# Optimization experiments

Measured on AMD Instinct MI355X. Metric: run time of the kernel, lower is better.

The kernel has to match this reference:

```python
import jax, jax.numpy as jnp
import numpy as np

B, N, M = 2, 1024, 512
D, H, DH = 1024, 16, 64          # features, heads, head dim (D == H*DH)
MID = H * DH
DC = 768                          # context_features
MULT = 4
EPS = 1e-5


def _ln(x, w, b):
    mu = jnp.mean(x, -1, keepdims=True)
    var = jnp.mean((x - mu) ** 2, -1, keepdims=True)
    return (x - mu) * jax.lax.rsqrt(var + EPS) * w + b


def _sincos(n, d):
    inv = 1.0 / (10000.0 ** (jnp.arange(0, d, 2, dtype=jnp.float32) / d))
    ang = jnp.arange(n, dtype=jnp.float32)[:, None] * inv[None, :]
    return jnp.sin(ang), jnp.cos(ang)


def _rope(x, sin, cos):
    # x: [B,H,N,DH]; sin/cos: [N, DH//2]; interleaved even/odd rotation
    s = sin[None, None]
    c = cos[None, None]
    xe = x[..., ::2]
    xo = x[..., 1::2]
    re = xe * c - xo * s
    ro = xe * s + xo * c
    return jnp.stack((re, ro), axis=-1).reshape(x.shape)


def _heads(t):
    b, n, _ = t.shape
    return t.reshape(b, n, H, DH).transpose(0, 2, 1, 3)


def _attn(xq, ctx, wq, wkv, wo, bo):
    q = _heads(xq @ wq)
    k, v = jnp.split(ctx @ wkv, 2, axis=-1)
    k = _heads(k)
    v = _heads(v)
    sq, cq = _sincos(q.shape[2], DH)
    sk, ck = _sincos(k.shape[2], DH)
    q = _rope(q, sq, cq)
    k = _rope(k, sk, ck)
    sim = jnp.einsum('bhnd,bhmd->bhnm', q, k) * (DH ** -0.5)
    a = jax.nn.softmax(sim, axis=-1)
    o = jnp.einsum('bhnm,bhmd->bhnd', a, v)
    o = o.transpose(0, 2, 1, 3).reshape(xq.shape[0], xq.shape[1], MID)
    return o @ wo + bo


def _adaln(x, c, lw, lb, gw, gb, bw, bb):
    g = (c @ gw + gb)[:, None, :]
    bt = (c @ bw + bb)[:, None, :]
    return _ln(x, lw, lb) * (1.0 + g) + bt


def setup_inputs() -> dict:
    ks = jax.random.split(jax.random.key(0), 24)
    s = 0.02
    inp = {
        'x': jax.random.normal(ks[0], (B, N, D), jnp.float32),
        'cond': jax.random.normal(ks[1], (B, D), jnp.float32),
        'context': jax.random.normal(ks[2], (B, M, DC), jnp.float32),
        # AdaLN (attn_mod) — reused for self- and cross-attention pre-norm
        'ln1_w': jnp.ones((D,), jnp.float32),
        'ln1_b': jnp.zeros((D,), jnp.float32),
        'g1_w': jax.random.normal(ks[3], (D, D), jnp.float32) * s,
        'g1_b': jnp.zeros((D,), jnp.float32),
        'b1_w': jax.random.normal(ks[4], (D, D), jnp.float32) * s,
        'b1_b': jnp.zeros((D,), jnp.float32),
        # AdaLN (ffn_mod)
        'ln2_w': jnp.ones((D,), jnp.float32),
        'ln2_b': jnp.zeros((D,), jnp.float32),
        'g2_w': jax.random.normal(ks[5], (D, D), jnp.float32) * s,
        'g2_b': jnp.zeros((D,), jnp.float32),
        'b2_w': jax.random.normal(ks[6], (D, D), jnp.float32) * s,
        'b2_b': jnp.zeros((D,), jnp.float32),
        # self-attention
        'sa_wq': jax.random.normal(ks[7], (D, MID), jnp.float32) * s,
        'sa_wkv': jax.random.normal(ks[8], (D, 2 * MID), jnp.float32) * s,
        'sa_wo': jax.random.normal(ks[9], (MID, D), jnp.float32) * s,
        'sa_bo': jnp.zeros((D,), jnp.float32),
        # cross-attention (context LayerNorm + projections)
        'ca_lnc_w': jnp.ones((DC,), jnp.float32),
        'ca_lnc_b': jnp.zeros((DC,), jnp.float32),
        'ca_wq': jax.random.normal(ks[10], (D, MID), jnp.float32) * s,
        'ca_wkv': jax.random.normal(ks[11], (DC, 2 * MID), jnp.float32) * s,
        'ca_wo': jax.random.normal(ks[12], (MID, D), jnp.float32) * s,
        'ca_bo': jnp.zeros((D,), jnp.float32),
        # FFN
        'ff_w1': jax.random.normal(ks[13], (D, MULT * D), jnp.float32) * s,
        'ff_b1': jnp.zeros((MULT * D,), jnp.float32),
        'ff_w2': jax.random.normal(ks[14], (MULT * D, D), jnp.float32) * s,
        'ff_b2': jnp.zeros((D,), jnp.float32),
    }
    return inp


def reference(x, cond, context,
              ln1_w, ln1_b, g1_w, g1_b, b1_w, b1_b,
              ln2_w, ln2_b, g2_w, g2_b, b2_w, b2_b,
              sa_wq, sa_wkv, sa_wo, sa_bo,
              ca_lnc_w, ca_lnc_b, ca_wq, ca_wkv, ca_wo, ca_bo,
              ff_w1, ff_b1, ff_w2, ff_b2):
    # self-attention with shared attn_mod AdaLN
    attn_in = _adaln(x, cond, ln1_w, ln1_b, g1_w, g1_b, b1_w, b1_b)
    x = _attn(attn_in, attn_in, sa_wq, sa_wkv, sa_wo, sa_bo) + x
    # cross-attention (attn_mod reused, context LayerNorm applied)
    cross_in = _adaln(x, cond, ln1_w, ln1_b, g1_w, g1_b, b1_w, b1_b)
    ctx_n = _ln(context, ca_lnc_w, ca_lnc_b)
    x = _attn(cross_in, ctx_n, ca_wq, ca_wkv, ca_wo, ca_bo) + x
    # FFN with ffn_mod AdaLN, exact GELU (torch default)
    ffn_in = _adaln(x, cond, ln2_w, ln2_b, g2_w, g2_b, b2_w, b2_b)
    h = jax.nn.gelu(ffn_in @ ff_w1 + ff_b1, approximate=False)
    x = h @ ff_w2 + ff_b2 + x
    return x
```

## Files before the change

kernel.cpp:

```cpp
#include <hip/hip_runtime.h>
#include <hip/hip_bf16.h>
#include <math.h>


typedef float f32x4 __attribute__((ext_vector_type(4)));
typedef __bf16 bf16x8 __attribute__((ext_vector_type(8)));
typedef __bf16 bf16x4 __attribute__((ext_vector_type(4)));
typedef __bf16 bf16x2 __attribute__((ext_vector_type(2)));

#define DEVI __device__ __forceinline__

DEVI void gload16(const void* g, void* l) {
  __builtin_amdgcn_global_load_lds((const __attribute__((address_space(1))) void*)g,
                                   (__attribute__((address_space(3))) void*)l, 16, 0, 0);
}

struct WtDesc {
  const float* src[8];
  __bf16* dst[8];
  int K[8], N[8];
  int tstart[9];
};

__global__ __launch_bounds__(256) void wt_all_kernel(WtDesc d) {
  __shared__ float tile[32][33];
  int blk = blockIdx.x;
  int e = 0;
#pragma unroll
  for (int i = 0; i < 7; ++i) e += (blk >= d.tstart[i + 1]) ? 1 : 0;
  int li = blk - d.tstart[e];
  const float* W = d.src[e];
  __bf16* WT = d.dst[e];
  int K = d.K[e], N = d.N[e];
  int ntx = N >> 5;
  int n0 = (li % ntx) * 32, k0 = (li / ntx) * 32;
  int tx = threadIdx.x & 31, ty = threadIdx.x >> 5;
#pragma unroll
  for (int i = 0; i < 4; ++i) {
    int k = ty + i * 8;
    tile[k][tx] = W[(size_t)(k0 + k) * N + n0 + tx];
  }
  __syncthreads();
#pragma unroll
  for (int i = 0; i < 4; ++i) {
    int n = ty + i * 8;
    WT[(size_t)(n0 + n) * K + k0 + tx] = (__bf16)tile[tx][n];
  }
}

__global__ __launch_bounds__(256) void mod_part_kernel(
    const float* __restrict__ cond,
    const float* __restrict__ g1w, const float* __restrict__ b1w,
    const float* __restrict__ g2w, const float* __restrict__ b2w,
    float* __restrict__ part) {
  __shared__ float sc[128];
  int dchunk = blockIdx.x, b = blockIdx.y;
  int mat = blockIdx.z >> 3, ks = blockIdx.z & 7;
  const float* W = (mat == 0) ? g1w : (mat == 1) ? b1w : (mat == 2) ? g2w : b2w;
  if (threadIdx.x < 128) sc[threadIdx.x] = cond[b * 1024 + ks * 128 + threadIdx.x];
  __syncthreads();
  int d = dchunk * 256 + threadIdx.x;
  const float* Wp = W + (size_t)(ks * 128) * 1024 + d;
  float acc = 0.f;
#pragma unroll 8
  for (int k = 0; k < 128; ++k) acc += sc[k] * Wp[(size_t)k * 1024];
  part[(size_t)(blockIdx.z * 2 + b) * 1024 + d] = acc;
}

__global__ __launch_bounds__(256) void mod_reduce_kernel(
    const float* __restrict__ part,
    const float* __restrict__ g1b, const float* __restrict__ b1b,
    const float* __restrict__ g2b, const float* __restrict__ b2b,
    float* __restrict__ mods) {
  int idx = blockIdx.x * 256 + threadIdx.x;
  int mat = idx >> 11, b = (idx >> 10) & 1, d = idx & 1023;
  float s = 0.f;
#pragma unroll
  for (int ks = 0; ks < 8; ++ks) s += part[(size_t)((mat * 8 + ks) * 2 + b) * 1024 + d];
  const float* Bv = (mat == 0) ? g1b : (mat == 1) ? b1b : (mat == 2) ? g2b : b2b;
  mods[(size_t)(mat * 2 + b) * 1024 + d] = s + Bv[d];
}

__global__ __launch_bounds__(256) void adaln_kernel(const float* __restrict__ X,
                                                    const float* __restrict__ lnw,
                                                    const float* __restrict__ lnb,
                                                    const float* __restrict__ mods,
                                                    int gi, int bi,
                                                    __bf16* __restrict__ out) {
  __shared__ float red[2][4];
  int row = blockIdx.x;
  int b = row >> 10;
  int t = threadIdx.x;
  const float4 xv = ((const float4*)(X + (size_t)row * 1024))[t];
  float s  = xv.x + xv.y + xv.z + xv.w;
  float s2 = xv.x * xv.x + xv.y * xv.y + xv.z * xv.z + xv.w * xv.w;
  int lane = t & 63, w = t >> 6;
#pragma unroll
  for (int off = 32; off > 0; off >>= 1) {
    s += __shfl_down(s, off);
    s2 += __shfl_down(s2, off);
  }
  if (lane == 0) { red[0][w] = s; red[1][w] = s2; }
  __syncthreads();
  s  = red[0][0] + red[0][1] + red[0][2] + red[0][3];
  s2 = red[1][0] + red[1][1] + red[1][2] + red[1][3];
  float mu = s * (1.0f / 1024.0f);
  float var = s2 * (1.0f / 1024.0f) - mu * mu;
  float rstd = rsqrtf(var + 1e-5f);
  const float4 wv = ((const float4*)lnw)[t];
  const float4 bv = ((const float4*)lnb)[t];
  const float4 gv = ((const float4*)(mods + (size_t)(gi * 2 + b) * 1024))[t];
  const float4 tv = ((const float4*)(mods + (size_t)(bi * 2 + b) * 1024))[t];
  bf16x4 ov;
  ov[0] = (__bf16)(((xv.x - mu) * rstd * wv.x + bv.x) * (1.0f + gv.x) + tv.x);
  ov[1] = (__bf16)(((xv.y - mu) * rstd * wv.y + bv.y) * (1.0f + gv.y) + tv.y);
  ov[2] = (__bf16)(((xv.z - mu) * rstd * wv.z + bv.z) * (1.0f + gv.z) + tv.z);
  ov[3] = (__bf16)(((xv.w - mu) * rstd * wv.w + bv.w) * (1.0f + gv.w) + tv.w);
  *(bf16x4*)(out + (size_t)row * 1024 + t * 4) = ov;
}

__global__ __launch_bounds__(256) void ctxln_kernel(const float* __restrict__ X,
                                                    const float* __restrict__ w,
                                                    const float* __restrict__ bias,
                                                    __bf16* __restrict__ out) {
  __shared__ float red[2][4];
  int row = blockIdx.x;
  int t = threadIdx.x;
  const float* xp = X + (size_t)row * 768;
  float v[3];
  float s = 0.f, s2 = 0.f;
#pragma unroll
  for (int i = 0; i < 3; ++i) {
    v[i] = xp[t + i * 256];
    s += v[i];
    s2 += v[i] * v[i];
  }
  int lane = t & 63, wv_ = t >> 6;
#pragma unroll
  for (int off = 32; off > 0; off >>= 1) {
    s += __shfl_down(s, off);
    s2 += __shfl_down(s2, off);
  }
  if (lane == 0) { red[0][wv_] = s; red[1][wv_] = s2; }
  __syncthreads();
  s  = red[0][0] + red[0][1] + red[0][2] + red[0][3];
  s2 = red[1][0] + red[1][1] + red[1][2] + red[1][3];
  float mu = s * (1.0f / 768.0f);
  float var = s2 * (1.0f / 768.0f) - mu * mu;
  float rstd = rsqrtf(var + 1e-5f);
#pragma unroll
  for (int i = 0; i < 3; ++i) {
    int c = t + i * 256;
    out[(size_t)row * 768 + c] = (__bf16)((v[i] - mu) * rstd * w[c] + bias[c]);
  }
}

__global__ __launch_bounds__(256) void rope_tbl_kernel(float2* __restrict__ tbl) {
  int idx = blockIdx.x * 256 + threadIdx.x;
  int n = idx >> 5, i = idx & 31;
  float inv = expf(-(float)(2 * i) * (1.0f / 64.0f) * 9.210340371976184f);
  float ang = (float)n * inv;
  tbl[idx] = make_float2(sinf(ang), cosf(ang));
}

__global__ __launch_bounds__(256) void vtb_kernel(const __bf16* __restrict__ Vb,
                                                  __bf16* __restrict__ VT, int Ntok) {
  __shared__ __bf16 tile[64][68];
  int bh = blockIdx.x, nt = blockIdx.y;
  int b = bh >> 4, h = bh & 15;
  int t = threadIdx.x;
  int tx = t & 15, ty = t >> 4;
#pragma unroll
  for (int i = 0; i < 4; ++i) {
    int n = ty + i * 16;
    bf16x4 v = *(const bf16x4*)(Vb + (size_t)(b * Ntok + nt * 64 + n) * 1024 + h * 64 + tx * 4);
#pragma unroll
    for (int j = 0; j < 4; ++j) tile[n][tx * 4 + j] = v[j];
  }
  __syncthreads();
#pragma unroll
  for (int i = 0; i < 4; ++i) {
    int d = ty + i * 16;
    bf16x4 o;
#pragma unroll
    for (int j = 0; j < 4; ++j) o[j] = tile[tx * 4 + j][d];
    *(bf16x4*)(VT + ((size_t)bh * 64 + d) * Ntok + nt * 64 + tx * 4) = o;
  }
}

template <int BM, int BN, int EPI, int DEPTH>
__global__ __launch_bounds__(256) void gemm3(const __bf16* __restrict__ A,
                                             const __bf16* __restrict__ BT,
                                             const float* __restrict__ bias,
                                             const float* __restrict__ res,
                                             void* __restrict__ outv,
                                             int M, int N, int K, int kslices,
                                             const float2* __restrict__ tbl,
                                             __bf16* __restrict__ Qro,
                                             __bf16* __restrict__ Kro,
                                             __bf16* __restrict__ Vbo,
                                             int Ntok) {
  constexpr int MI = BM / 32, NI = BN / 32;
  constexpr int NBUF = DEPTH + 1;
  constexpr int LPT = BM / 64 + BN / 64;
  __shared__ __bf16 sA[NBUF][BM * 32];
  __shared__ __bf16 sB[NBUF][BN * 32];
  const int t = threadIdx.x;
  const int w = t >> 6, lane = t & 63;
  const int lr = lane & 15, lg = lane >> 4;
  const int fxor = (lr >> 1) & 3;
  int nwg = gridDim.x * gridDim.y * gridDim.z;
  int flat = blockIdx.x + gridDim.x * (blockIdx.y + gridDim.y * blockIdx.z);
  flat = (flat & 7) * (nwg >> 3) + (flat >> 3);
  const int bm = flat % gridDim.x;
  int rest = flat / gridDim.x;
  const int bn = rest % gridDim.y;
  const int bz = rest / gridDim.y;
  const int wm = (w >> 1) * (BM / 2), wn = (w & 1) * (BN / 2);
  const int kper = K / kslices;
  const int k0 = bz * kper;
  const int nsteps = kper / 32;
  f32x4 acc[MI][NI] = {};

  auto stage = [&](int buf, int kt) {
#pragma unroll
    for (int i = 0; i < BM / 64; ++i) {
      int e8 = i * 256 + t;
      int row = e8 >> 2, c = e8 & 3;
      int scol = (c ^ ((row >> 1) & 3)) << 3;
      gload16(A + (size_t)(bm * BM + row) * K + kt + scol, &sA[buf][e8 * 8]);
    }
#pragma unroll
    for (int i = 0; i < BN / 64; ++i) {
      int e8 = i * 256 + t;
      int row = e8 >> 2, c = e8 & 3;
      int scol = (c ^ ((row >> 1) & 3)) << 3;
      gload16(BT + (size_t)(bn * BN + row) * K + kt + scol, &sB[buf][e8 * 8]);
    }
  };

  auto compute = [&](int buf) {
    bf16x8 af[MI], bfr[NI];
#pragma unroll
    for (int mi = 0; mi < MI; ++mi)
      af[mi] = *(const bf16x8*)(&sA[buf][(wm + mi * 16 + lr) * 32 + ((lg ^ fxor) << 3)]);
#pragma unroll
    for (int ni = 0; ni < NI; ++ni)
      bfr[ni] = *(const bf16x8*)(&sB[buf][(wn + ni * 16 + lr) * 32 + ((lg ^ fxor) << 3)]);
#pragma unroll
    for (int mi = 0; mi < MI; ++mi)
#pragma unroll
      for (int ni = 0; ni < NI; ++ni)
        acc[mi][ni] = __builtin_amdgcn_mfma_f32_16x16x32_bf16(af[mi], bfr[ni], acc[mi][ni], 0, 0, 0);
  };

#pragma unroll
  for (int i = 0; i < DEPTH; ++i) stage(i, k0 + i * 32);

  int it = 0;
  for (; it < nsteps - (DEPTH - 1); ++it) {
    asm volatile("s_waitcnt vmcnt(%0)" :: "n"((DEPTH - 1) * LPT) : "memory");
    __builtin_amdgcn_s_barrier();
    __builtin_amdgcn_sched_barrier(0);
    if (it + DEPTH < nsteps) stage((it + DEPTH) % NBUF, k0 + (it + DEPTH) * 32);
    compute(it % NBUF);
  }
  asm volatile("s_waitcnt vmcnt(0)" ::: "memory");
  __builtin_amdgcn_s_barrier();
  __builtin_amdgcn_sched_barrier(0);
  for (; it < nsteps; ++it) compute(it % NBUF);

#pragma unroll
  for (int mi = 0; mi < MI; ++mi) {
    int row = bm * BM + wm + mi * 16 + lg * 4;
#pragma unroll
    for (int ni = 0; ni < NI; ++ni) {
      int col = bn * BN + wn + ni * 16 + lr;
#pragma unroll
      for (int r = 0; r < 4; ++r) {
        float v = acc[mi][ni][r];
        int erow = row + r;
        size_t off = (size_t)erow * N + col;
        if (EPI == 0) {
          ((float*)outv)[off] = v;
        } else if (EPI == 1) {
          ((float*)outv)[off] = v + bias[col] + res[off];
        } else if (EPI == 2) {
          float xg = v + bias[col];
          ((__bf16*)outv)[off] = (__bf16)(0.5f * xg * (1.0f + erff(xg * 0.7071067811865475f)));
        } else if (EPI == 3) {
          ((float*)outv)[(size_t)bz * M * N + off] = v;
        } else if (EPI == 4) {
          float ov = __shfl_xor(v, 1);
          int b = erow >> 10, n = erow & 1023;
          if (col < 2048) {
            int h = (col >> 6) & 15, dh = col & 63;
            float2 sc = tbl[n * 32 + (dh >> 1)];
            float rv = (lr & 1) ? (ov * sc.x + v * sc.y) : (v * sc.y - ov * sc.x);
            __bf16* dst;
            if (col < 1024) { rv *= 0.125f; dst = Qro; } else dst = Kro;
            dst[((size_t)(b * 16 + h) * Ntok + n) * 64 + dh] = (__bf16)rv;
          } else {
            Vbo[(size_t)erow * 1024 + (col - 2048)] = (__bf16)v;
          }
        } else if (EPI == 5) {
          float ov = __shfl_xor(v, 1);
          int b = erow >> 10, n = erow & 1023;
          int h = col >> 6, dh = col & 63;
          float2 sc = tbl[n * 32 + (dh >> 1)];
          float rv = ((lr & 1) ? (ov * sc.x + v * sc.y) : (v * sc.y - ov * sc.x)) * 0.125f;
          Qro[((size_t)(b * 16 + h) * Ntok + n) * 64 + dh] = (__bf16)rv;
        } else {
          float ov = __shfl_xor(v, 1);
          int b = erow >> 9, n = erow & 511;
          if (col < 1024) {
            int h = col >> 6, dh = col & 63;
            float2 sc = tbl[n * 32 + (dh >> 1)];
            float rv = (lr & 1) ? (ov * sc.x + v * sc.y) : (v * sc.y - ov * sc.x);
            Kro[((size_t)(b * 16 + h) * Ntok + n) * 64 + dh] = (__bf16)rv;
          } else {
            Vbo[(size_t)erow * 1024 + (col - 1024)] = (__bf16)v;
          }
        }
      }
    }
  }
}

__global__ __launch_bounds__(256) void ff2red_kernel(const float* __restrict__ part,
                                                     const float* __restrict__ bias,
                                                     const float* __restrict__ res,
                                                     float* __restrict__ out, int MN, int N) {
  int idx = blockIdx.x * 256 + threadIdx.x;
  float4 p0 = ((const float4*)part)[idx];
  float4 p1 = ((const float4*)(part + MN))[idx];
  float4 rr = ((const float4*)res)[idx];
  int colb = (idx * 4) & (N - 1);
  float4 bb = *(const float4*)(bias + colb);
  float4 o;
  o.x = p0.x + p1.x + bb.x + rr.x;
  o.y = p0.y + p1.y + bb.y + rr.y;
  o.z = p0.z + p1.z + bb.z + rr.z;
  o.w = p0.w + p1.w + bb.w + rr.w;
  ((float4*)out)[idx] = o;
}

template <int KITERS>
__global__ __launch_bounds__(256) void attn_kernel(const __bf16* __restrict__ Qr,
                                                   const __bf16* __restrict__ Kr,
                                                   const __bf16* __restrict__ VT,
                                                   __bf16* __restrict__ O,
                                                   int Nq, int Nk) {
  __shared__ __bf16 sK[2][64 * 64];
  __shared__ __bf16 sV[2][64 * 64];
  __shared__ __bf16 Pl[4][16 * 64];
  const int t = threadIdx.x, w = t >> 6, lane = t & 63;
  const int lr = lane & 15, lg = lane >> 4;
  const int lsrc = lane & 48;
  const int swz = (lr & 7) << 3;
  int flat = blockIdx.x + (blockIdx.y << 4);
  flat = (flat & 7) * 64 + (flat >> 3);
  const int bh = flat >> 4;
  const int q0 = (flat & 15) * 64 + w * 16;
  const int b = bh >> 4, h = bh & 15;

  auto stage = [&](int buf, int kt) {
#pragma unroll
    for (int i = 0; i < 2; ++i) {
      int e8 = i * 256 + t;
      int row = e8 >> 3, col8 = e8 & 7;
      int scol = (col8 ^ (row & 7)) << 3;
      gload16(Kr + ((size_t)bh * Nk + kt + row) * 64 + scol, &sK[buf][e8 * 8]);
      gload16(VT + ((size_t)bh * 64 + row) * Nk + kt + scol, &sV[buf][e8 * 8]);
    }
  };

  bf16x8 qf[2];
#pragma unroll
  for (int kh = 0; kh < 2; ++kh)
    qf[kh] = *(const bf16x8*)(Qr + ((size_t)bh * Nq + q0 + lr) * 64 + kh * 32 + lg * 8);
  f32x4 accO[4] = {};
  float m = -INFINITY, l = 0.f;

  stage(0, 0);
  __syncthreads();
  int cur = 0;
#pragma unroll
  for (int it = 0; it < KITERS; ++it) {
    if (it + 1 < KITERS) stage(cur ^ 1, (it + 1) * 64);
    f32x4 s[4] = {};
#pragma unroll
    for (int nf = 0; nf < 4; ++nf) {
      int r = nf * 16 + lr;
#pragma unroll
      for (int kh = 0; kh < 2; ++kh) {
        bf16x8 kf = *(const bf16x8*)(&sK[cur][r * 64 + (((kh * 4 + lg) ^ (lr & 7)) << 3)]);
        s[nf] = __builtin_amdgcn_mfma_f32_16x16x32_bf16(kf, qf[kh], s[nf], 0, 0, 0);
      }
    }
    float p[16];
#pragma unroll
    for (int j = 0; j < 16; ++j) p[j] = s[j >> 2][j & 3];
    float pm = p[0];
#pragma unroll
    for (int j = 1; j < 16; ++j) pm = fmaxf(pm, p[j]);
    pm = fmaxf(pm, __shfl_xor(pm, 16));
    pm = fmaxf(pm, __shfl_xor(pm, 32));
    if (!__all(pm <= m + 8.f)) {
      float mnew = fmaxf(m, pm);
      float resc = __expf(m - mnew);
      float rq[4];
#pragma unroll
      for (int r = 0; r < 4; ++r) rq[r] = __shfl(resc, lsrc | (lg * 4 + r));
#pragma unroll
      for (int df = 0; df < 4; ++df)
#pragma unroll
        for (int r = 0; r < 4; ++r) accO[df][r] *= rq[r];
      l *= resc;
      m = mnew;
    }
    float rs = 0.f;
#pragma unroll
    for (int j = 0; j < 16; ++j) { p[j] = __expf(p[j] - m); rs += p[j]; }
    rs += __shfl_xor(rs, 16);
    rs += __shfl_xor(rs, 32);
    l += rs;
#pragma unroll
    for (int nf = 0; nf < 4; ++nf)
#pragma unroll
      for (int jj = 0; jj < 2; ++jj) {
        int k = nf * 16 + lg * 4 + 2 * jj;
        bf16x2 pk;
        pk[0] = (__bf16)p[nf * 4 + 2 * jj];
        pk[1] = (__bf16)p[nf * 4 + 2 * jj + 1];
        *(bf16x2*)(&Pl[w][lr * 64 + (k ^ swz)]) = pk;
      }
    bf16x8 pa0 = *(const bf16x8*)(&Pl[w][lr * 64 + ((lg * 8) ^ swz)]);
    bf16x8 pa1 = *(const bf16x8*)(&Pl[w][lr * 64 + ((32 + lg * 8) ^ swz)]);
#pragma unroll
    for (int df = 0; df < 4; ++df) {
      int d = df * 16 + lr;
      bf16x8 vf0 = *(const bf16x8*)(&sV[cur][d * 64 + ((lg ^ (lr & 7)) << 3)]);
      bf16x8 vf1 = *(const bf16x8*)(&sV[cur][d * 64 + (((4 + lg) ^ (lr & 7)) << 3)]);
      accO[df] = __builtin_amdgcn_mfma_f32_16x16x32_bf16(pa0, vf0, accO[df], 0, 0, 0);
      accO[df] = __builtin_amdgcn_mfma_f32_16x16x32_bf16(pa1, vf1, accO[df], 0, 0, 0);
    }
    __syncthreads();
    cur ^= 1;
  }
  float lq[4];
#pragma unroll
  for (int r = 0; r < 4; ++r) lq[r] = __shfl(l, lsrc | (lg * 4 + r));
#pragma unroll
  for (int r = 0; r < 4; ++r) {
    float inv = 1.0f / lq[r];
    int n = q0 + lg * 4 + r;
#pragma unroll
    for (int df = 0; df < 4; ++df)
      O[(size_t)(b * 1024 + n) * 1024 + h * 64 + df * 16 + lr] = (__bf16)(accO[df][r] * inv);
  }
}

extern "C" void kernel_launch(void* const* d_in, const int* in_sizes, int n_in,
                              void* d_out, int out_size, void* d_ws, size_t ws_size,
                              hipStream_t stream) {
  (void)in_sizes; (void)n_in; (void)out_size; (void)ws_size;
  const float* x       = (const float*)d_in[0];
  const float* cond    = (const float*)d_in[1];
  const float* ctx     = (const float*)d_in[2];
  const float* ln1_w   = (const float*)d_in[3];
  const float* ln1_b   = (const float*)d_in[4];
  const float* g1_w    = (const float*)d_in[5];
  const float* g1_b    = (const float*)d_in[6];
  const float* b1_w    = (const float*)d_in[7];
  const float* b1_b    = (const float*)d_in[8];
  const float* ln2_w   = (const float*)d_in[9];
  const float* ln2_b   = (const float*)d_in[10];
  const float* g2_w    = (const float*)d_in[11];
  const float* g2_b    = (const float*)d_in[12];
  const float* b2_w    = (const float*)d_in[13];
  const float* b2_b    = (const float*)d_in[14];
  const float* sa_wq   = (const float*)d_in[15];
  const float* sa_wkv  = (const float*)d_in[16];
  const float* sa_wo   = (const float*)d_in[17];
  const float* sa_bo   = (const float*)d_in[18];
  const float* ca_lnc_w = (const float*)d_in[19];
  const float* ca_lnc_b = (const float*)d_in[20];
  const float* ca_wq   = (const float*)d_in[21];
  const float* ca_wkv  = (const float*)d_in[22];
  const float* ca_wo   = (const float*)d_in[23];
  const float* ca_bo   = (const float*)d_in[24];
  const float* ff_w1   = (const float*)d_in[25];
  const float* ff_b1   = (const float*)d_in[26];
  const float* ff_w2   = (const float*)d_in[27];
  const float* ff_b2   = (const float*)d_in[28];
  float* out = (float*)d_out;

  char* ws = (char*)d_ws;
  size_t o = 0;
  auto alloc = [&](size_t bytes) {
    void* p = ws + o;
    o += (bytes + 255) & ~(size_t)255;
    return p;
  };

  __bf16* wqT   = (__bf16*)alloc(1024ull * 1024 * 2);
  __bf16* wkvT  = (__bf16*)alloc(2048ull * 1024 * 2);
  __bf16* woT   = (__bf16*)alloc(1024ull * 1024 * 2);
  __bf16* cwqT  = (__bf16*)alloc(1024ull * 1024 * 2);
  __bf16* cwkvT = (__bf16*)alloc(2048ull * 768 * 2);
  __bf16* cwoT  = (__bf16*)alloc(1024ull * 1024 * 2);
  __bf16* ff1T  = (__bf16*)alloc(4096ull * 1024 * 2);
  __bf16* ff2T  = (__bf16*)alloc(1024ull * 4096 * 2);
  float*  mods  = (float*)alloc(4ull * 2 * 1024 * 4);
  float2* tbl   = (float2*)alloc(1024ull * 32 * 8);
  __bf16* ain   = (__bf16*)alloc(2048ull * 1024 * 2);
  float*  Qf    = (float*)alloc(2048ull * 1024 * 4);
  float*  KVf   = (float*)alloc(2048ull * 2048 * 4);
  __bf16* ctxn  = (__bf16*)alloc(1024ull * 768 * 2);
  __bf16* Qr    = (__bf16*)alloc(2048ull * 1024 * 2);
  __bf16* Kr    = (__bf16*)alloc(2048ull * 1024 * 2);
  __bf16* VTb   = (__bf16*)alloc(2048ull * 1024 * 2);
  __bf16* Ob    = (__bf16*)alloc(2048ull * 1024 * 2);
  float*  x1    = (float*)alloc(2048ull * 1024 * 4);
  float*  x2    = (float*)alloc(2048ull * 1024 * 4);
  __bf16* hb    = (__bf16*)KVf;
  float*  pbuf  = (float*)Qr;
  float*  mpart = (float*)Qf;
  __bf16* Vb    = (__bf16*)Qf;

  WtDesc wd;
  const float* srcs[8] = {sa_wq, sa_wkv, sa_wo, ca_wq, ca_wkv, ca_wo, ff_w1, ff_w2};
  __bf16* dsts[8] = {wqT, wkvT, woT, cwqT, cwkvT, cwoT, ff1T, ff2T};
  int Ks[8] = {1024, 1024, 1024, 1024, 768, 1024, 1024, 4096};
  int Ns[8] = {1024, 2048, 1024, 1024, 2048, 1024, 4096, 1024};
  int cum = 0;
  for (int i = 0; i < 8; ++i) {
    wd.src[i] = srcs[i]; wd.dst[i] = dsts[i]; wd.K[i] = Ks[i]; wd.N[i] = Ns[i];
    wd.tstart[i] = cum;
    cum += (Ks[i] >> 5) * (Ns[i] >> 5);
  }
  wd.tstart[8] = cum;
  wt_all_kernel<<<cum, 256, 0, stream>>>(wd);
  rope_tbl_kernel<<<128, 256, 0, stream>>>(tbl);
  mod_part_kernel<<<dim3(4, 2, 32), 256, 0, stream>>>(cond, g1_w, b1_w, g2_w, b2_w, mpart);
  mod_reduce_kernel<<<32, 256, 0, stream>>>(mpart, g1_b, b1_b, g2_b, b2_b, mods);

  adaln_kernel<<<2048, 256, 0, stream>>>(x, ln1_w, ln1_b, mods, 0, 1, ain);
  gemm3<128, 128, 4, 3><<<dim3(16, 24), 256, 0, stream>>>(ain, wqT, nullptr, nullptr, nullptr,
                                                          2048, 3072, 1024, 1, tbl, Qr, Kr, Vb, 1024);
  vtb_kernel<<<dim3(32, 16), 256, 0, stream>>>(Vb, VTb, 1024);
  attn_kernel<16><<<dim3(16, 32), 256, 0, stream>>>(Qr, Kr, VTb, Ob, 1024, 1024);
  gemm3<128, 64, 1, 3><<<dim3(16, 16), 256, 0, stream>>>(Ob, woT, sa_bo, x, x1,
                                                         2048, 1024, 1024, 1, nullptr, nullptr, nullptr, nullptr, 0);

  adaln_kernel<<<2048, 256, 0, stream>>>(x1, ln1_w, ln1_b, mods, 0, 1, ain);
  ctxln_kernel<<<1024, 256, 0, stream>>>(ctx, ca_lnc_w, ca_lnc_b, ctxn);
  gemm3<128, 64, 5, 3><<<dim3(16, 16), 256, 0, stream>>>(ain, cwqT, nullptr, nullptr, nullptr,
                                                         2048, 1024, 1024, 1, tbl, Qr, nullptr, nullptr, 1024);
  gemm3<128, 64, 6, 3><<<dim3(8, 32), 256, 0, stream>>>(ctxn, cwkvT, nullptr, nullptr, nullptr,
                                                        1024, 2048, 768, 1, tbl, nullptr, Kr, Vb, 512);
  vtb_kernel<<<dim3(32, 8), 256, 0, stream>>>(Vb, VTb, 512);
  attn_kernel<8><<<dim3(16, 32), 256, 0, stream>>>(Qr, Kr, VTb, Ob, 1024, 512);
  gemm3<128, 64, 1, 3><<<dim3(16, 16), 256, 0, stream>>>(Ob, cwoT, ca_bo, x1, x2,
                                                         2048, 1024, 1024, 1, nullptr, nullptr, nullptr, nullptr, 0);

  adaln_kernel<<<2048, 256, 0, stream>>>(x2, ln2_w, ln2_b, mods, 2, 3, ain);
  gemm3<128, 128, 2, 3><<<dim3(16, 32), 256, 0, stream>>>(ain, ff1T, ff_b1, nullptr, hb,
                                                          2048, 4096, 1024, 1, nullptr, nullptr, nullptr, nullptr, 0);
  gemm3<128, 64, 3, 3><<<dim3(16, 16, 2), 256, 0, stream>>>(hb, ff2T, nullptr, nullptr, pbuf,
                                                            2048, 1024, 4096, 2, nullptr, nullptr, nullptr, nullptr, 0);
  ff2red_kernel<<<2048, 256, 0, stream>>>(pbuf, ff_b2, x2, out, 2048 * 1024, 1024);
}
```

Baseline: 272.1 us.

## Merge prep kernels, fuse cross-attn Q and KV GEMMs, shrink GEMM tiles

```diff
diff --git a/kernel.cpp b/kernel.cpp
--- a/kernel.cpp
+++ b/kernel.cpp
@@ -22,49 +22,60 @@
   int tstart[9];
 };
 
-__global__ __launch_bounds__(256) void wt_all_kernel(WtDesc d) {
-  __shared__ float tile[32][33];
+__global__ __launch_bounds__(256) void prep_kernel(WtDesc d,
+                                                   float2* __restrict__ tbl,
+                                                   const float* __restrict__ cond,
+                                                   const float* __restrict__ g1w,
+                                                   const float* __restrict__ b1w,
+                                                   const float* __restrict__ g2w,
+                                                   const float* __restrict__ b2w,
+                                                   float* __restrict__ part) {
+  __shared__ float smem[32][33];
   int blk = blockIdx.x;
-  int e = 0;
-#pragma unroll
-  for (int i = 0; i < 7; ++i) e += (blk >= d.tstart[i + 1]) ? 1 : 0;
-  int li = blk - d.tstart[e];
-  const float* W = d.src[e];
-  __bf16* WT = d.dst[e];
-  int K = d.K[e], N = d.N[e];
-  int ntx = N >> 5;
-  int n0 = (li % ntx) * 32, k0 = (li / ntx) * 32;
-  int tx = threadIdx.x & 31, ty = threadIdx.x >> 5;
-#pragma unroll
-  for (int i = 0; i < 4; ++i) {
-    int k = ty + i * 8;
-    tile[k][tx] = W[(size_t)(k0 + k) * N + n0 + tx];
-  }
-  __syncthreads();
-#pragma unroll
-  for (int i = 0; i < 4; ++i) {
-    int n = ty + i * 8;
-    WT[(size_t)(n0 + n) * K + k0 + tx] = (__bf16)tile[tx][n];
-  }
-}
-
-__global__ __launch_bounds__(256) void mod_part_kernel(
-    const float* __restrict__ cond,
-    const float* __restrict__ g1w, const float* __restrict__ b1w,
-    const float* __restrict__ g2w, const float* __restrict__ b2w,
-    float* __restrict__ part) {
-  __shared__ float sc[128];
-  int dchunk = blockIdx.x, b = blockIdx.y;
-  int mat = blockIdx.z >> 3, ks = blockIdx.z & 7;
-  const float* W = (mat == 0) ? g1w : (mat == 1) ? b1w : (mat == 2) ? g2w : b2w;
-  if (threadIdx.x < 128) sc[threadIdx.x] = cond[b * 1024 + ks * 128 + threadIdx.x];
-  __syncthreads();
-  int d = dchunk * 256 + threadIdx.x;
-  const float* Wp = W + (size_t)(ks * 128) * 1024 + d;
-  float acc = 0.f;
+  int wtend = d.tstart[8];
+  if (blk < wtend) {
+    int e = 0;
+#pragma unroll
+    for (int i = 0; i < 7; ++i) e += (blk >= d.tstart[i + 1]) ? 1 : 0;
+    int li = blk - d.tstart[e];
+    const float* W = d.src[e];
+    __bf16* WT = d.dst[e];
+    int K = d.K[e], N = d.N[e];
+    int ntx = N >> 5;
+    int n0 = (li % ntx) * 32, k0 = (li / ntx) * 32;
+    int tx = threadIdx.x & 31, ty = threadIdx.x >> 5;
+#pragma unroll
+    for (int i = 0; i < 4; ++i) {
+      int k = ty + i * 8;
+      smem[k][tx] = W[(size_t)(k0 + k) * N + n0 + tx];
+    }
+    __syncthreads();
+#pragma unroll
+    for (int i = 0; i < 4; ++i) {
+      int n = ty + i * 8;
+      WT[(size_t)(n0 + n) * K + k0 + tx] = (__bf16)smem[tx][n];
+    }
+  } else if (blk < wtend + 128) {
+    int idx = (blk - wtend) * 256 + threadIdx.x;
+    int n = idx >> 5, i = idx & 31;
+    float inv = expf(-(float)(2 * i) * (1.0f / 64.0f) * 9.210340371976184f);
+    float ang = (float)n * inv;
+    tbl[idx] = make_float2(sinf(ang), cosf(ang));
+  } else {
+    int f = blk - wtend - 128;
+    int dchunk = f & 3, b = (f >> 2) & 1, z = f >> 3;
+    int mat = z >> 3, ks = z & 7;
+    const float* W = (mat == 0) ? g1w : (mat == 1) ? b1w : (mat == 2) ? g2w : b2w;
+    float* sc = &smem[0][0];
+    if (threadIdx.x < 128) sc[threadIdx.x] = cond[b * 1024 + ks * 128 + threadIdx.x];
+    __syncthreads();
+    int dd = dchunk * 256 + threadIdx.x;
+    const float* Wp = W + (size_t)(ks * 128) * 1024 + dd;
+    float acc = 0.f;
 #pragma unroll 8
-  for (int k = 0; k < 128; ++k) acc += sc[k] * Wp[(size_t)k * 1024];
-  part[(size_t)(blockIdx.z * 2 + b) * 1024 + d] = acc;
+    for (int k = 0; k < 128; ++k) acc += sc[k] * Wp[(size_t)k * 1024];
+    part[(size_t)(z * 2 + b) * 1024 + dd] = acc;
+  }
 }
 
 __global__ __launch_bounds__(256) void mod_reduce_kernel(
@@ -153,14 +164,6 @@
     int c = t + i * 256;
     out[(size_t)row * 768 + c] = (__bf16)((v[i] - mu) * rstd * w[c] + bias[c]);
   }
-}
-
-__global__ __launch_bounds__(256) void rope_tbl_kernel(float2* __restrict__ tbl) {
-  int idx = blockIdx.x * 256 + threadIdx.x;
-  int n = idx >> 5, i = idx & 31;
-  float inv = expf(-(float)(2 * i) * (1.0f / 64.0f) * 9.210340371976184f);
-  float ang = (float)n * inv;
-  tbl[idx] = make_float2(sinf(ang), cosf(ang));
 }
 
 __global__ __launch_bounds__(256) void vtb_kernel(const __bf16* __restrict__ Vb,
@@ -303,21 +306,112 @@
           } else {
             Vbo[(size_t)erow * 1024 + (col - 2048)] = (__bf16)v;
           }
-        } else if (EPI == 5) {
-          float ov = __shfl_xor(v, 1);
+        }
+      }
+    }
+  }
+}
+
+__global__ __launch_bounds__(256) void gemm_cross(const __bf16* __restrict__ Aq,
+                                                  const __bf16* __restrict__ Bq,
+                                                  const __bf16* __restrict__ Akv,
+                                                  const __bf16* __restrict__ Bkv,
+                                                  const float2* __restrict__ tbl,
+                                                  __bf16* __restrict__ Qro,
+                                                  __bf16* __restrict__ Kro,
+                                                  __bf16* __restrict__ Vbo) {
+  constexpr int BM = 128, BN = 64, DEPTH = 3, NBUF = 4, LPT = 3;
+  constexpr int MI = 4, NI = 2;
+  __shared__ __bf16 sA[NBUF][BM * 32];
+  __shared__ __bf16 sB[NBUF][BN * 32];
+  const int t = threadIdx.x;
+  const int w = t >> 6, lane = t & 63;
+  const int lr = lane & 15, lg = lane >> 4;
+  const int fxor = (lr >> 1) & 3;
+  int flat = blockIdx.x;
+  flat = (flat & 7) * 64 + (flat >> 3);
+  const bool isq = flat < 256;
+  const __bf16* A  = isq ? Aq : Akv;
+  const __bf16* BT = isq ? Bq : Bkv;
+  const int K = isq ? 1024 : 768;
+  int lf = isq ? flat : flat - 256;
+  const int bm = isq ? (lf & 15) : (lf & 7);
+  const int bn = isq ? (lf >> 4) : (lf >> 3);
+  const int wm = (w >> 1) * 64, wn = (w & 1) * 32;
+  const int nsteps = K >> 5;
+  f32x4 acc[MI][NI] = {};
+
+  auto stage = [&](int buf, int kt) {
+#pragma unroll
+    for (int i = 0; i < 2; ++i) {
+      int e8 = i * 256 + t;
+      int row = e8 >> 2, c = e8 & 3;
+      int scol = (c ^ ((row >> 1) & 3)) << 3;
+      gload16(A + (size_t)(bm * BM + row) * K + kt + scol, &sA[buf][e8 * 8]);
+    }
+    {
+      int e8 = t;
+      int row = e8 >> 2, c = e8 & 3;
+      int scol = (c ^ ((row >> 1) & 3)) << 3;
+      gload16(BT + (size_t)(bn * BN + row) * K + kt + scol, &sB[buf][e8 * 8]);
+    }
+  };
+
+  auto compute = [&](int buf) {
+    bf16x8 af[MI], bfr[NI];
+#pragma unroll
+    for (int mi = 0; mi < MI; ++mi)
+      af[mi] = *(const bf16x8*)(&sA[buf][(wm + mi * 16 + lr) * 32 + ((lg ^ fxor) << 3)]);
+#pragma unroll
+    for (int ni = 0; ni < NI; ++ni)
+      bfr[ni] = *(const bf16x8*)(&sB[buf][(wn + ni * 16 + lr) * 32 + ((lg ^ fxor) << 3)]);
+#pragma unroll
+    for (int mi = 0; mi < MI; ++mi)
+#pragma unroll
+      for (int ni = 0; ni < NI; ++ni)
+        acc[mi][ni] = __builtin_amdgcn_mfma_f32_16x16x32_bf16(af[mi], bfr[ni], acc[mi][ni], 0, 0, 0);
+  };
+
+#pragma unroll
+  for (int i = 0; i < DEPTH; ++i) stage(i, i * 32);
+
+  int it = 0;
+  for (; it < nsteps - (DEPTH - 1); ++it) {
+    asm volatile("s_waitcnt vmcnt(%0)" :: "n"((DEPTH - 1) * LPT) : "memory");
+    __builtin_amdgcn_s_barrier();
+    __builtin_amdgcn_sched_barrier(0);
+    if (it + DEPTH < nsteps) stage((it + DEPTH) % NBUF, (it + DEPTH) * 32);
+    compute(it % NBUF);
+  }
+  asm volatile("s_waitcnt vmcnt(0)" ::: "memory");
+  __builtin_amdgcn_s_barrier();
+  __builtin_amdgcn_sched_barrier(0);
+  for (; it < nsteps; ++it) compute(it % NBUF);
+
+#pragma unroll
+  for (int mi = 0; mi < MI; ++mi) {
+    int row = bm * BM + wm + mi * 16 + lg * 4;
+#pragma unroll
+    for (int ni = 0; ni < NI; ++ni) {
+      int col = bn * BN + wn + ni * 16 + lr;
+#pragma unroll
+      for (int r = 0; r < 4; ++r) {
+        float v = acc[mi][ni][r];
+        int erow = row + r;
+        float ov = __shfl_xor(v, 1);
+        if (isq) {
           int b = erow >> 10, n = erow & 1023;
           int h = col >> 6, dh = col & 63;
           float2 sc = tbl[n * 32 + (dh >> 1)];
           float rv = ((lr & 1) ? (ov * sc.x + v * sc.y) : (v * sc.y - ov * sc.x)) * 0.125f;
-          Qro[((size_t)(b * 16 + h) * Ntok + n) * 64 + dh] = (__bf16)rv;
+          Qro[((size_t)(b * 16 + h) * 1024 + n) * 64 + dh] = (__bf16)rv;
         } else {
-          float ov = __shfl_xor(v, 1);
           int b = erow >> 9, n = erow & 511;
           if (col < 1024) {
             int h = col >> 6, dh = col & 63;
             float2 sc = tbl[n * 32 + (dh >> 1)];
             float rv = (lr & 1) ? (ov * sc.x + v * sc.y) : (v * sc.y - ov * sc.x);
-            Kro[((size_t)(b * 16 + h) * Ntok + n) * 64 + dh] = (__bf16)rv;
+            Kro[((size_t)(b * 16 + h) * 512 + n) * 64 + dh] = (__bf16)rv;
           } else {
             Vbo[(size_t)erow * 1024 + (col - 1024)] = (__bf16)v;
           }
@@ -541,14 +635,12 @@
     cum += (Ks[i] >> 5) * (Ns[i] >> 5);
   }
   wd.tstart[8] = cum;
-  wt_all_kernel<<<cum, 256, 0, stream>>>(wd);
-  rope_tbl_kernel<<<128, 256, 0, stream>>>(tbl);
-  mod_part_kernel<<<dim3(4, 2, 32), 256, 0, stream>>>(cond, g1_w, b1_w, g2_w, b2_w, mpart);
+  prep_kernel<<<cum + 128 + 256, 256, 0, stream>>>(wd, tbl, cond, g1_w, b1_w, g2_w, b2_w, mpart);
   mod_reduce_kernel<<<32, 256, 0, stream>>>(mpart, g1_b, b1_b, g2_b, b2_b, mods);
 
   adaln_kernel<<<2048, 256, 0, stream>>>(x, ln1_w, ln1_b, mods, 0, 1, ain);
-  gemm3<128, 128, 4, 3><<<dim3(16, 24), 256, 0, stream>>>(ain, wqT, nullptr, nullptr, nullptr,
-                                                          2048, 3072, 1024, 1, tbl, Qr, Kr, Vb, 1024);
+  gemm3<128, 64, 4, 3><<<dim3(16, 48), 256, 0, stream>>>(ain, wqT, nullptr, nullptr, nullptr,
+                                                         2048, 3072, 1024, 1, tbl, Qr, Kr, Vb, 1024);
   vtb_kernel<<<dim3(32, 16), 256, 0, stream>>>(Vb, VTb, 1024);
   attn_kernel<16><<<dim3(16, 32), 256, 0, stream>>>(Qr, Kr, VTb, Ob, 1024, 1024);
   gemm3<128, 64, 1, 3><<<dim3(16, 16), 256, 0, stream>>>(Ob, woT, sa_bo, x, x1,
@@ -556,18 +648,15 @@
 
   adaln_kernel<<<2048, 256, 0, stream>>>(x1, ln1_w, ln1_b, mods, 0, 1, ain);
   ctxln_kernel<<<1024, 256, 0, stream>>>(ctx, ca_lnc_w, ca_lnc_b, ctxn);
-  gemm3<128, 64, 5, 3><<<dim3(16, 16), 256, 0, stream>>>(ain, cwqT, nullptr, nullptr, nullptr,
-                                                         2048, 1024, 1024, 1, tbl, Qr, nullptr, nullptr, 1024);
-  gemm3<128, 64, 6, 3><<<dim3(8, 32), 256, 0, stream>>>(ctxn, cwkvT, nullptr, nullptr, nullptr,
-                                                        1024, 2048, 768, 1, tbl, nullptr, Kr, Vb, 512);
+  gemm_cross<<<512, 256, 0, stream>>>(ain, cwqT, ctxn, cwkvT, tbl, Qr, Kr, Vb);
   vtb_kernel<<<dim3(32, 8), 256, 0, stream>>>(Vb, VTb, 512);
   attn_kernel<8><<<dim3(16, 32), 256, 0, stream>>>(Qr, Kr, VTb, Ob, 1024, 512);
   gemm3<128, 64, 1, 3><<<dim3(16, 16), 256, 0, stream>>>(Ob, cwoT, ca_bo, x1, x2,
                                                          2048, 1024, 1024, 1, nullptr, nullptr, nullptr, nullptr, 0);
 
   adaln_kernel<<<2048, 256, 0, stream>>>(x2, ln2_w, ln2_b, mods, 2, 3, ain);
-  gemm3<128, 128, 2, 3><<<dim3(16, 32), 256, 0, stream>>>(ain, ff1T, ff_b1, nullptr, hb,
-                                                          2048, 4096, 1024, 1, nullptr, nullptr, nullptr, nullptr, 0);
+  gemm3<128, 64, 2, 3><<<dim3(16, 64), 256, 0, stream>>>(ain, ff1T, ff_b1, nullptr, hb,
+                                                         2048, 4096, 1024, 1, nullptr, nullptr, nullptr, nullptr, 0);
   gemm3<128, 64, 3, 3><<<dim3(16, 16, 2), 256, 0, stream>>>(hb, ff2T, nullptr, nullptr, pbuf,
                                                             2048, 1024, 4096, 2, nullptr, nullptr, nullptr, nullptr, 0);
   ff2red_kernel<<<2048, 256, 0, stream>>>(pbuf, ff_b2, x2, out, 2048 * 1024, 1024);
```

Result: faster. 257.6 us (-5.3%).
